# Performance work log

Hardware: AMD Instinct MI355X
Metric: run time of the kernel (lower is better)

## Reference

```python
import jax, jax.numpy as jnp
import numpy as np

B, N, K, D, H = 4, 8192, 16, 128, 4
DK = D // H  # key_dim = num_hiddens // num_heads
NEG_INF = -1e9


def setup_inputs() -> dict:
    key = jax.random.key(0)
    ks = jax.random.split(key, 16)
    s = 1.0 / np.sqrt(D)
    return {
        "vertex_feat": jax.random.normal(ks[0], (B, N, D), dtype=jnp.float32),
        "neighbors_idx": jax.random.randint(ks[1], (B, N, K), 0, N, dtype=jnp.int32),
        "valid_lens": jax.random.randint(ks[2], (B, N), 0, K, dtype=jnp.int32),
        # MultiHeadAttention projections (keras EinsumDense with bias)
        "Wq": (jax.random.normal(ks[3], (D, H, DK)) * s).astype(jnp.float32),
        "bq": jnp.zeros((H, DK), jnp.float32),
        "Wk": (jax.random.normal(ks[4], (D, H, DK)) * s).astype(jnp.float32),
        "bk": jnp.zeros((H, DK), jnp.float32),
        "Wv": (jax.random.normal(ks[5], (D, H, DK)) * s).astype(jnp.float32),
        "bv": jnp.zeros((H, DK), jnp.float32),
        "Wo": (jax.random.normal(ks[6], (H, DK, D)) * s).astype(jnp.float32),
        "bo": jnp.zeros((D,), jnp.float32),
        # MLP: Dense(D, relu) -> Dense(D)
        "W1": (jax.random.normal(ks[7], (D, D)) * s).astype(jnp.float32),
        "b1": jnp.zeros((D,), jnp.float32),
        "W2": (jax.random.normal(ks[8], (D, D)) * s).astype(jnp.float32),
        "b2": jnp.zeros((D,), jnp.float32),
    }


def reference(vertex_feat, neighbors_idx, valid_lens,
              Wq, bq, Wk, bk, Wv, bv, Wo, bo, W1, b1, W2, b2):
    # query: [B, N, 1, D]; gathered neighbors (batch_dims=1): [B, N, K, D]
    q = vertex_feat[:, :, None, :]
    neigh = jax.vmap(lambda vf, idx: vf[idx])(vertex_feat, neighbors_idx)
    value = jnp.concatenate([q, neigh], axis=2)  # [B, N, K+1, D]

    # per-head projections
    qh = jnp.einsum('bnqd,dhk->bnqhk', q, Wq) + bq      # [B,N,1,H,DK]
    kh = jnp.einsum('bnsd,dhk->bnshk', value, Wk) + bk  # [B,N,K+1,H,DK]
    vh = jnp.einsum('bnsd,dhk->bnshk', value, Wv) + bv

    # attention over the neighbor axis (attention_axes=(2,))
    scores = jnp.einsum('bnqhk,bnshk->bnhqs', qh, kh) / np.sqrt(DK)  # [B,N,H,1,K+1]
    # mask: positions < valid_lens + 1 (self + valid neighbors)
    pos = jnp.arange(K + 1)[None, None, :]                # [1,1,K+1]
    mask = pos < (valid_lens + 1)[:, :, None]             # [B,N,K+1] bool
    scores = scores + jnp.where(mask, 0.0, NEG_INF)[:, :, None, None, :]
    attn = jax.nn.softmax(scores, axis=-1)                # [B,N,H,1,K+1]

    ctx = jnp.einsum('bnhqs,bnshk->bnqhk', attn, vh)      # [B,N,1,H,DK]
    out = jnp.einsum('bnqhk,hkd->bnqd', ctx, Wo) + bo     # [B,N,1,D]
    out = out[:, :, 0, :]                                  # squeeze -> [B,N,D]

    # MLP (dropout inactive at inference)
    h = jax.nn.relu(out @ W1 + b1)
    new_vertex_feat = h @ W2 + b2
    return new_vertex_feat
```

## Files before the change

kernel.cpp:

```cpp
#include <hip/hip_runtime.h>
#include <math.h>

#define BB 4
#define NN 8192
#define KNB 16
#define DD 128
#define SS 17
#define M_TOT (BB*NN)
#define WPAD 136

typedef __attribute__((ext_vector_type(8))) short          bf8;
typedef __attribute__((ext_vector_type(4))) float          f4;
typedef __attribute__((ext_vector_type(4))) unsigned short u16x4;

static __device__ __forceinline__ unsigned short f2bf(float f) {
    unsigned u = __builtin_bit_cast(unsigned, f);
    u += 0x7fffu + ((u >> 16) & 1u);
    return (unsigned short)(u >> 16);
}
static __device__ __forceinline__ float bf2f_s(short h) {
    return __builtin_bit_cast(float, (unsigned)(unsigned short)h << 16);
}

__global__ __launch_bounds__(256) void cvt_wT(
    const float* __restrict__ Wq, const float* __restrict__ Wk,
    const float* __restrict__ Wv, const float* __restrict__ Wo,
    const float* __restrict__ W1, const float* __restrict__ W2,
    unsigned short* __restrict__ out)
{
    int m = blockIdx.x >> 4;
    const float* src = (m == 0) ? Wq : (m == 1) ? Wk : (m == 2) ? Wv
                     : (m == 3) ? Wo : (m == 4) ? W1 : W2;
    unsigned short* dst = out + m * 16384;
    int o = (blockIdx.x & 15) * 1024 + threadIdx.x * 4;
    int n = o >> 7, k = o & 127;
    u16x4 r;
    #pragma unroll
    for (int i = 0; i < 4; ++i) r[i] = f2bf(src[(size_t)(k + i) * 128 + n]);
    *(u16x4*)(dst + o) = r;
}

__global__ __launch_bounds__(256) void qkv_kernel(
    const float* __restrict__ X, const unsigned short* __restrict__ WtT,
    const float* __restrict__ bq, const float* __restrict__ bk,
    const float* __restrict__ bv,
    unsigned short* __restrict__ qh, unsigned short* __restrict__ kv)
{
    __shared__ unsigned short Xs[64 * WPAD];
    __shared__ unsigned short Wb[128 * WPAD];

    const int tid  = threadIdx.x;
    const int row0 = blockIdx.x * 64;

    {
        const float4* Xg = (const float4*)(X + (size_t)row0 * DD);
        #pragma unroll
        for (int i = 0; i < 8; ++i) {
            int idx = tid + i * 256;
            int r = idx >> 5, c4 = idx & 31;
            float4 v = Xg[idx];
            u16x4 u;
            u[0] = f2bf(v.x); u[1] = f2bf(v.y); u[2] = f2bf(v.z); u[3] = f2bf(v.w);
            *(u16x4*)(Xs + r * WPAD + c4 * 4) = u;
        }
    }
    #pragma unroll
    for (int i = 0; i < 8; ++i) {
        int c = tid + i * 256;
        int n = c >> 4, k8 = c & 15;
        *(bf8*)(Wb + n * WPAD + k8 * 8) = ((const bf8*)WtT)[c];
    }

    const int lane = tid & 63, wv = tid >> 6;
    const int ln = lane & 15, quad = lane >> 4;
    __syncthreads();

    bf8 afr[4];
    #pragma unroll
    for (int s = 0; s < 4; ++s)
        afr[s] = *(const bf8*)(Xs + (wv * 16 + ln) * WPAD + s * 32 + quad * 8);

    const float* biases[3] = { bq, bk, bv };
    unsigned short* outs[3] = { qh, kv, kv + 128 };
    const int strides[3] = { 128, 256, 256 };

    #pragma unroll 1
    for (int g = 0; g < 3; ++g) {
        if (g > 0) {
            __syncthreads();
            const bf8* Wn = (const bf8*)(WtT + g * 16384);
            #pragma unroll
            for (int i = 0; i < 8; ++i) {
                int c = tid + i * 256;
                int n = c >> 4, k8 = c & 15;
                *(bf8*)(Wb + n * WPAD + k8 * 8) = Wn[c];
            }
            __syncthreads();
        }

        f4 acc[8] = {};
        #pragma unroll
        for (int t = 0; t < 8; ++t) {
            bf8 bfr[4];
            #pragma unroll
            for (int s = 0; s < 4; ++s)
                bfr[s] = *(const bf8*)(Wb + (t * 16 + ln) * WPAD + s * 32 + quad * 8);
            #pragma unroll
            for (int s = 0; s < 4; ++s)
                acc[t] = __builtin_amdgcn_mfma_f32_16x16x32_bf16(afr[s], bfr[s], acc[t], 0, 0, 0);
        }

        const float* bias = biases[g];
        unsigned short* Y = outs[g];
        const int st = strides[g];
        #pragma unroll
        for (int t = 0; t < 8; ++t) {
            int col = t * 16 + ln;
            float bc = bias[col];
            #pragma unroll
            for (int r = 0; r < 4; ++r) {
                int row = row0 + wv * 16 + quad * 4 + r;
                Y[(size_t)row * st + col] = f2bf(acc[t][r] + bc);
            }
        }
    }
}

__global__ __launch_bounds__(256) void attn_kernel(
    const unsigned short* __restrict__ Qh, const unsigned short* __restrict__ KV,
    const int* __restrict__ nbr, const int* __restrict__ vlen,
    unsigned short* __restrict__ Ctx)
{
    const int tid  = threadIdx.x;
    const int vloc = tid >> 5;
    const int sp   = (tid >> 4) & 1;
    const int ln16 = tid & 15;
    const int blk  = blockIdx.x;
    const int b    = (blk & 7) >> 1;
    const int j    = ((blk >> 3) << 1) | (blk & 1);
    const int v    = b * NN + j * 8 + vloc;
    const int len  = vlen[v];

    bf8 q8 = *(const bf8*)(Qh + (size_t)v * DD + ln16 * 8);
    float qf[8];
    #pragma unroll
    for (int i = 0; i < 8; ++i) qf[i] = bf2f_s(q8[i]);

    int rows[9];
    {
        const int4* np = (const int4*)(nbr + (size_t)v * KNB);
        if (sp == 0) {
            rows[0] = v;
            int4 a = np[0], c = np[1];
            rows[1] = b * NN + a.x; rows[2] = b * NN + a.y;
            rows[3] = b * NN + a.z; rows[4] = b * NN + a.w;
            rows[5] = b * NN + c.x; rows[6] = b * NN + c.y;
            rows[7] = b * NN + c.z; rows[8] = b * NN + c.w;
        } else {
            int4 a = np[2], c = np[3];
            rows[0] = b * NN + a.x; rows[1] = b * NN + a.y;
            rows[2] = b * NN + a.z; rows[3] = b * NN + a.w;
            rows[4] = b * NN + c.x; rows[5] = b * NN + c.y;
            rows[6] = b * NN + c.z; rows[7] = b * NN + c.w;
            rows[8] = v;
        }
    }
    const int s0 = sp * 9;

    float sc[9];
    #pragma unroll
    for (int i = 0; i < 9; ++i) {
        bf8 k8 = *(const bf8*)(KV + (size_t)rows[i] * 256 + ln16 * 8);
        float p = 0.f;
        #pragma unroll
        for (int d = 0; d < 8; ++d) p = fmaf(qf[d], bf2f_s(k8[d]), p);
        p += __shfl_xor(p, 1, 4);
        p += __shfl_xor(p, 2, 4);
        sc[i] = (s0 + i <= len) ? p * 0.17677669529663687f : -1.0e9f;
    }

    float m = sc[0];
    #pragma unroll
    for (int i = 1; i < 9; ++i) m = fmaxf(m, sc[i]);
    m = fmaxf(m, __shfl_xor(m, 16));
    float sum = 0.f;
    #pragma unroll
    for (int i = 0; i < 9; ++i) {
        float e = __expf(sc[i] - m);
        sc[i] = e;
        sum += e;
    }
    sum += __shfl_xor(sum, 16);
    const float inv = 1.f / sum;

    float acc[8] = {};
    #pragma unroll
    for (int i = 0; i < 9; ++i) {
        bf8 v8 = *(const bf8*)(KV + (size_t)rows[i] * 256 + 128 + ln16 * 8);
        float w = sc[i] * inv;
        #pragma unroll
        for (int d = 0; d < 8; ++d) acc[d] = fmaf(w, bf2f_s(v8[d]), acc[d]);
    }
    #pragma unroll
    for (int d = 0; d < 8; ++d) acc[d] += __shfl_xor(acc[d], 16);

    if (sp == 0) {
        bf8 r;
        #pragma unroll
        for (int d = 0; d < 8; ++d) r[d] = (short)f2bf(acc[d]);
        *(bf8*)(Ctx + (size_t)v * DD + ln16 * 8) = r;
    }
}

__global__ __launch_bounds__(256) void ffn_kernel(
    const unsigned short* __restrict__ Ctxg, const unsigned short* __restrict__ WtT3,
    const float* __restrict__ bo, const float* __restrict__ b1,
    const float* __restrict__ b2, float* __restrict__ Out)
{
    __shared__ unsigned short Ct[64 * WPAD];
    __shared__ unsigned short Wb[128 * WPAD];

    const int tid  = threadIdx.x;
    const int row0 = blockIdx.x * 64;

    {
        const bf8* Cg = (const bf8*)(Ctxg + (size_t)row0 * DD);
        #pragma unroll
        for (int i = 0; i < 4; ++i) {
            int idx = tid + i * 256;
            int r = idx >> 4, c8 = idx & 15;
            *(bf8*)(Ct + r * WPAD + c8 * 8) = Cg[idx];
        }
    }
    #pragma unroll
    for (int i = 0; i < 8; ++i) {
        int c = tid + i * 256;
        int n = c >> 4, k8 = c & 15;
        *(bf8*)(Wb + n * WPAD + k8 * 8) = ((const bf8*)WtT3)[c];
    }

    const int lane = tid & 63, wv = tid >> 6;
    const int ln = lane & 15, quad = lane >> 4;
    const float* biases[3] = { bo, b1, b2 };
    __syncthreads();

    #pragma unroll 1
    for (int g = 0; g < 3; ++g) {
        bf8 afr[4];
        #pragma unroll
        for (int s = 0; s < 4; ++s)
            afr[s] = *(const bf8*)(Ct + (wv * 16 + ln) * WPAD + s * 32 + quad * 8);

        f4 acc[8] = {};
        #pragma unroll
        for (int t = 0; t < 8; ++t) {
            bf8 bfr[4];
            #pragma unroll
            for (int s = 0; s < 4; ++s)
                bfr[s] = *(const bf8*)(Wb + (t * 16 + ln) * WPAD + s * 32 + quad * 8);
            #pragma unroll
            for (int s = 0; s < 4; ++s)
                acc[t] = __builtin_amdgcn_mfma_f32_16x16x32_bf16(afr[s], bfr[s], acc[t], 0, 0, 0);
        }

        __syncthreads();

        const float* bias = biases[g];
        if (g == 2) {
            #pragma unroll
            for (int t = 0; t < 8; ++t) {
                int col = t * 16 + ln;
                float bc = bias[col];
                #pragma unroll
                for (int r = 0; r < 4; ++r) {
                    int row = row0 + wv * 16 + quad * 4 + r;
                    Out[(size_t)row * DD + col] = acc[t][r] + bc;
                }
            }
        } else {
            const bf8* Wn = (const bf8*)(WtT3 + (g + 1) * 16384);
            #pragma unroll
            for (int i = 0; i < 8; ++i) {
                int c = tid + i * 256;
                int n = c >> 4, k8 = c & 15;
                *(bf8*)(Wb + n * WPAD + k8 * 8) = Wn[c];
            }
            #pragma unroll
            for (int t = 0; t < 8; ++t) {
                int col = t * 16 + ln;
                float bc = bias[col];
                #pragma unroll
                for (int r = 0; r < 4; ++r) {
                    int rloc = wv * 16 + quad * 4 + r;
                    float vv = acc[t][r] + bc;
                    if (g == 1) vv = fmaxf(vv, 0.f);
                    Ct[rloc * WPAD + col] = f2bf(vv);
                }
            }
            __syncthreads();
        }
    }
}

extern "C" void kernel_launch(void* const* d_in, const int* in_sizes, int n_in,
                              void* d_out, int out_size, void* d_ws, size_t ws_size,
                              hipStream_t stream)
{
    const float* vf   = (const float*)d_in[0];
    const int*   nbr  = (const int*)  d_in[1];
    const int*   vlen = (const int*)  d_in[2];
    const float* Wq   = (const float*)d_in[3];
    const float* bq   = (const float*)d_in[4];
    const float* Wk   = (const float*)d_in[5];
    const float* bk   = (const float*)d_in[6];
    const float* Wv   = (const float*)d_in[7];
    const float* bv   = (const float*)d_in[8];
    const float* Wo   = (const float*)d_in[9];
    const float* bo   = (const float*)d_in[10];
    const float* W1   = (const float*)d_in[11];
    const float* b1   = (const float*)d_in[12];
    const float* W2   = (const float*)d_in[13];
    const float* b2   = (const float*)d_in[14];

    float* out = (float*)d_out;

    const size_t SZ = (size_t)M_TOT * DD;
    unsigned short* WtT = (unsigned short*)d_ws;
    unsigned short* qh  = WtT + 6 * 16384;
    unsigned short* kv  = qh + SZ;
    unsigned short* ctx = kv + 2 * SZ;

    cvt_wT<<<96, 256, 0, stream>>>(Wq, Wk, Wv, Wo, W1, W2, WtT);

    qkv_kernel<<<M_TOT / 64, 256, 0, stream>>>(vf, WtT, bq, bk, bv, qh, kv);

    attn_kernel<<<M_TOT / 8, 256, 0, stream>>>(qh, kv, nbr, vlen, ctx);

    ffn_kernel<<<M_TOT / 64, 256, 0, stream>>>(ctx, WtT + 3 * 16384, bo, b1, b2, out);
}
```

Baseline: 136.0 us.

## Load GEMM operands directly from global memory and batch gather loads in attention

```diff
diff --git a/kernel.cpp b/kernel.cpp
--- a/kernel.cpp
+++ b/kernel.cpp
@@ -46,39 +46,24 @@
     const float* __restrict__ bv,
     unsigned short* __restrict__ qh, unsigned short* __restrict__ kv)
 {
-    __shared__ unsigned short Xs[64 * WPAD];
-    __shared__ unsigned short Wb[128 * WPAD];
-
     const int tid  = threadIdx.x;
     const int row0 = blockIdx.x * 64;
-
-    {
-        const float4* Xg = (const float4*)(X + (size_t)row0 * DD);
-        #pragma unroll
-        for (int i = 0; i < 8; ++i) {
-            int idx = tid + i * 256;
-            int r = idx >> 5, c4 = idx & 31;
-            float4 v = Xg[idx];
-            u16x4 u;
-            u[0] = f2bf(v.x); u[1] = f2bf(v.y); u[2] = f2bf(v.z); u[3] = f2bf(v.w);
-            *(u16x4*)(Xs + r * WPAD + c4 * 4) = u;
-        }
-    }
-    #pragma unroll
-    for (int i = 0; i < 8; ++i) {
-        int c = tid + i * 256;
-        int n = c >> 4, k8 = c & 15;
-        *(bf8*)(Wb + n * WPAD + k8 * 8) = ((const bf8*)WtT)[c];
-    }
-
     const int lane = tid & 63, wv = tid >> 6;
     const int ln = lane & 15, quad = lane >> 4;
-    __syncthreads();
-
+
+    const int arow = row0 + wv * 16 + ln;
     bf8 afr[4];
     #pragma unroll
-    for (int s = 0; s < 4; ++s)
-        afr[s] = *(const bf8*)(Xs + (wv * 16 + ln) * WPAD + s * 32 + quad * 8);
+    for (int s = 0; s < 4; ++s) {
+        const float4* xp = (const float4*)(X + (size_t)arow * DD + s * 32 + quad * 8);
+        float4 x0 = xp[0], x1 = xp[1];
+        bf8 a;
+        a[0] = (short)f2bf(x0.x); a[1] = (short)f2bf(x0.y);
+        a[2] = (short)f2bf(x0.z); a[3] = (short)f2bf(x0.w);
+        a[4] = (short)f2bf(x1.x); a[5] = (short)f2bf(x1.y);
+        a[6] = (short)f2bf(x1.z); a[7] = (short)f2bf(x1.w);
+        afr[s] = a;
+    }
 
     const float* biases[3] = { bq, bk, bv };
     unsigned short* outs[3] = { qh, kv, kv + 128 };
@@ -86,25 +71,14 @@
 
     #pragma unroll 1
     for (int g = 0; g < 3; ++g) {
-        if (g > 0) {
-            __syncthreads();
-            const bf8* Wn = (const bf8*)(WtT + g * 16384);
-            #pragma unroll
-            for (int i = 0; i < 8; ++i) {
-                int c = tid + i * 256;
-                int n = c >> 4, k8 = c & 15;
-                *(bf8*)(Wb + n * WPAD + k8 * 8) = Wn[c];
-            }
-            __syncthreads();
-        }
-
+        const unsigned short* Wg = WtT + g * 16384;
         f4 acc[8] = {};
         #pragma unroll
         for (int t = 0; t < 8; ++t) {
             bf8 bfr[4];
             #pragma unroll
             for (int s = 0; s < 4; ++s)
-                bfr[s] = *(const bf8*)(Wb + (t * 16 + ln) * WPAD + s * 32 + quad * 8);
+                bfr[s] = *(const bf8*)(Wg + (size_t)(t * 16 + ln) * 128 + s * 32 + quad * 8);
             #pragma unroll
             for (int s = 0; s < 4; ++s)
                 acc[t] = __builtin_amdgcn_mfma_f32_16x16x32_bf16(afr[s], bfr[s], acc[t], 0, 0, 0);
@@ -167,17 +141,26 @@
     }
     const int s0 = sp * 9;
 
+    bf8 k8[9];
+    #pragma unroll
+    for (int i = 0; i < 9; ++i)
+        k8[i] = *(const bf8*)(KV + (size_t)rows[i] * 256 + ln16 * 8);
+
     float sc[9];
     #pragma unroll
     for (int i = 0; i < 9; ++i) {
-        bf8 k8 = *(const bf8*)(KV + (size_t)rows[i] * 256 + ln16 * 8);
         float p = 0.f;
         #pragma unroll
-        for (int d = 0; d < 8; ++d) p = fmaf(qf[d], bf2f_s(k8[d]), p);
+        for (int d = 0; d < 8; ++d) p = fmaf(qf[d], bf2f_s(k8[i][d]), p);
         p += __shfl_xor(p, 1, 4);
         p += __shfl_xor(p, 2, 4);
         sc[i] = (s0 + i <= len) ? p * 0.17677669529663687f : -1.0e9f;
     }
+
+    bf8 v8[9];
+    #pragma unroll
+    for (int i = 0; i < 9; ++i)
+        v8[i] = *(const bf8*)(KV + (size_t)rows[i] * 256 + 128 + ln16 * 8);
 
     float m = sc[0];
     #pragma unroll
@@ -196,10 +179,9 @@
     float acc[8] = {};
     #pragma unroll
     for (int i = 0; i < 9; ++i) {
-        bf8 v8 = *(const bf8*)(KV + (size_t)rows[i] * 256 + 128 + ln16 * 8);
         float w = sc[i] * inv;
         #pragma unroll
-        for (int d = 0; d < 8; ++d) acc[d] = fmaf(w, bf2f_s(v8[d]), acc[d]);
+        for (int d = 0; d < 8; ++d) acc[d] = fmaf(w, bf2f_s(v8[i][d]), acc[d]);
     }
     #pragma unroll
     for (int d = 0; d < 8; ++d) acc[d] += __shfl_xor(acc[d], 16);
@@ -218,7 +200,6 @@
     const float* __restrict__ b2, float* __restrict__ Out)
 {
     __shared__ unsigned short Ct[64 * WPAD];
-    __shared__ unsigned short Wb[128 * WPAD];
 
     const int tid  = threadIdx.x;
     const int row0 = blockIdx.x * 64;
@@ -232,12 +213,6 @@
             *(bf8*)(Ct + r * WPAD + c8 * 8) = Cg[idx];
         }
     }
-    #pragma unroll
-    for (int i = 0; i < 8; ++i) {
-        int c = tid + i * 256;
-        int n = c >> 4, k8 = c & 15;
-        *(bf8*)(Wb + n * WPAD + k8 * 8) = ((const bf8*)WtT3)[c];
-    }
 
     const int lane = tid & 63, wv = tid >> 6;
     const int ln = lane & 15, quad = lane >> 4;
@@ -251,19 +226,18 @@
         for (int s = 0; s < 4; ++s)
             afr[s] = *(const bf8*)(Ct + (wv * 16 + ln) * WPAD + s * 32 + quad * 8);
 
+        const unsigned short* Wg = WtT3 + g * 16384;
         f4 acc[8] = {};
         #pragma unroll
         for (int t = 0; t < 8; ++t) {
             bf8 bfr[4];
             #pragma unroll
             for (int s = 0; s < 4; ++s)
-                bfr[s] = *(const bf8*)(Wb + (t * 16 + ln) * WPAD + s * 32 + quad * 8);
+                bfr[s] = *(const bf8*)(Wg + (size_t)(t * 16 + ln) * 128 + s * 32 + quad * 8);
             #pragma unroll
             for (int s = 0; s < 4; ++s)
                 acc[t] = __builtin_amdgcn_mfma_f32_16x16x32_bf16(afr[s], bfr[s], acc[t], 0, 0, 0);
         }
-
-        __syncthreads();
 
         const float* bias = biases[g];
         if (g == 2) {
@@ -278,13 +252,7 @@
                 }
             }
         } else {
-            const bf8* Wn = (const bf8*)(WtT3 + (g + 1) * 16384);
-            #pragma unroll
-            for (int i = 0; i < 8; ++i) {
-                int c = tid + i * 256;
-                int n = c >> 4, k8 = c & 15;
-                *(bf8*)(Wb + n * WPAD + k8 * 8) = Wn[c];
-            }
+            __syncthreads();
             #pragma unroll
             for (int t = 0; t < 8; ++t) {
                 int col = t * 16 + ln;
```

Result: slower. 170.3 us (+25.2%).
